# Performance work log

Measured on AMD Instinct MI355X. Metric: run time of the kernel, lower is better.

Reference implementation:

```python
import jax, jax.numpy as jnp
import numpy as np

# Config (matches init_kwargs)
N, P, K, DIMS = 16, 1024, 16, 3
C_IN, C_MID, C_OUT, DM = 64, 64, 128, 4
C_CAT = C_MID + C_IN          # channels entering depthwise-separable conv
KK = K * K
BN_EPS = 1e-5


def setup_inputs() -> dict:
    key = jax.random.key(0)
    ks = jax.random.split(key, 24)
    s = 0.05  # small init scale for weights
    inp = {
        # forward args
        "rep_pt": jax.random.normal(ks[0], (N, P, DIMS), jnp.float32),
        "pts":    jax.random.normal(ks[1], (N, P, K, DIMS), jnp.float32),
        "fts":    jax.random.normal(ks[2], (N, P, K, C_IN), jnp.float32),
        # dense1 / dense2 (point lifting MLP), weights stored (in, out)
        "w1": jax.random.normal(ks[3], (DIMS, C_MID), jnp.float32) * s,
        "b1": jnp.zeros((C_MID,), jnp.float32),
        "w2": jax.random.normal(ks[4], (C_MID, C_MID), jnp.float32) * s,
        "b2": jnp.zeros((C_MID,), jnp.float32),
        # conv1: Conv2d(dims, K*K, (1,K)); weight (KK, dims, K)
        "wc1": jax.random.normal(ks[5], (KK, DIMS, K), jnp.float32) * s,
        "bc1": jnp.zeros((KK,), jnp.float32),
        # x_dense1 (ELU) and x_dense2 (no activation)
        "wx1": jax.random.normal(ks[6], (KK, KK), jnp.float32) * s,
        "bx1": jnp.zeros((KK,), jnp.float32),
        "wx2": jax.random.normal(ks[7], (KK, KK), jnp.float32) * s,
        "bx2": jnp.zeros((KK,), jnp.float32),
        # depthwise Conv2d(C_CAT, C_CAT*DM, (1,K), groups=C_CAT): weight (C_CAT, DM, K)
        "wdw": jax.random.normal(ks[8], (C_CAT, DM, K), jnp.float32) * s,
        "bdw": jnp.zeros((C_CAT * DM,), jnp.float32),
        # pointwise Conv2d(C_CAT*DM, C_OUT, 1): weight stored (C_CAT*DM, C_OUT)
        "wpw": jax.random.normal(ks[9], (C_CAT * DM, C_OUT), jnp.float32) * s,
        "bpw": jnp.zeros((C_OUT,), jnp.float32),
        # BatchNorm2d(C_OUT) in eval mode (running stats)
        "bn_gamma": jnp.ones((C_OUT,), jnp.float32),
        "bn_beta":  jnp.zeros((C_OUT,), jnp.float32),
        "bn_mean":  jax.random.normal(ks[10], (C_OUT,), jnp.float32) * 0.1,
        "bn_var":   jax.random.uniform(ks[11], (C_OUT,), jnp.float32, 0.5, 1.5),
    }
    return inp


def reference(rep_pt, pts, fts, w1, b1, w2, b2, wc1, bc1, wx1, bx1, wx2, bx2,
              wdw, bdw, wpw, bpw, bn_gamma, bn_beta, bn_mean, bn_var):
    elu = jax.nn.elu
    n, p, k = pts.shape[0], pts.shape[1], pts.shape[2]

    # localize points around representative point: (N,P,K,dims)
    pts_local = pts - rep_pt[:, :, None, :]

    # lift coordinates to C_mid features (two Dense+ELU)
    h = elu(pts_local @ w1 + b1)
    h = elu(h @ w2 + b2)
    fts_cat = jnp.concatenate([h, fts], axis=-1)  # (N,P,K,C_CAT)

    # learned X-transform: conv1 over the K neighbors -> (N,P,K*K)
    X = elu(jnp.einsum('npkd,odk->npo', pts_local, wc1) + bc1)
    X = elu(X @ wx1 + bx1)
    X = X @ wx2 + bx2            # x_dense2: no activation
    X = X.reshape(n, p, k, k)    # (N,P,K,K)

    # apply X-transform to concatenated features
    fts_X = jnp.einsum('npij,npjc->npic', X, fts_cat)  # (N,P,K,C_CAT)

    # depthwise conv (kernel (1,K), groups=C_CAT, depth multiplier DM)
    # torch grouped-conv channel order: out channel o = c*DM + d
    dw = jnp.einsum('npkc,cdk->npcd', fts_X, wdw).reshape(n, p, -1) + bdw
    # pointwise 1x1 conv -> C_OUT, then ELU
    y = elu(dw @ wpw + bpw)      # (N,P,C_OUT)
    # BatchNorm2d in eval mode (per-channel affine with running stats)
    y = (y - bn_mean) * (bn_gamma / jnp.sqrt(bn_var + BN_EPS)) + bn_beta
    return y                     # (N,P,C_OUT)
```

## Files before the change

### kernel.cpp

```cpp
#include <hip/hip_runtime.h>

#define NPTS 16384
#define MPB  16
#define NTHR 256
#define WS_NEEDED 401408u

typedef __attribute__((ext_vector_type(8))) short bf16x8;
typedef __attribute__((ext_vector_type(4))) float f32x4;

__device__ __forceinline__ unsigned short f2bf(float x) {
    unsigned u = __float_as_uint(x);
    return (unsigned short)((u + 0x7FFFu + ((u >> 16) & 1u)) >> 16);
}
__device__ __forceinline__ float bf2f(unsigned short h) {
    return __uint_as_float(((unsigned)h) << 16);
}
__device__ __forceinline__ float elu_f(float x) {
    return x > 0.f ? x : (__expf(x) - 1.f);
}

__device__ __forceinline__ bf16x8 load_bfrag(const float* __restrict__ W, int N,
                                             int kt, int nt, int lane) {
    int k0  = kt * 32 + ((lane >> 4) << 3);
    int col = nt * 16 + (lane & 15);
    const float* s = W + k0 * N + col;
    bf16x8 r;
#pragma unroll
    for (int j = 0; j < 8; j++) r[j] = (short)f2bf(s[j * N]);
    return r;
}

__global__ void pack_weights(const float* __restrict__ w2,
                             const float* __restrict__ wx1,
                             const float* __restrict__ wx2,
                             const float* __restrict__ wpw,
                             unsigned short* __restrict__ dst) {
    int gid  = blockIdx.x * 256 + threadIdx.x;
    int frag = gid >> 6, lane = gid & 63;
    const float* src; int N, fl;
    if      (frag <   8) { src = w2;  N =  64; fl = frag;       }
    else if (frag < 136) { src = wx1; N = 256; fl = frag - 8;   }
    else if (frag < 264) { src = wx2; N = 256; fl = frag - 136; }
    else                 { src = wpw; N = 128; fl = frag - 264; }
    int NT  = N >> 4;
    int kt  = fl / NT, nt = fl - kt * NT;
    int k0  = kt * 32 + (lane >> 4) * 8;
    int col = nt * 16 + (lane & 15);
    const float* s = src + k0 * N + col;
    unsigned v[4];
#pragma unroll
    for (int u = 0; u < 4; u++) {
        unsigned lo = f2bf(s[(2 * u) * N]);
        unsigned hi = f2bf(s[(2 * u + 1) * N]);
        v[u] = lo | (hi << 16);
    }
    *(uint4*)&dst[gid * 8] = make_uint4(v[0], v[1], v[2], v[3]);
}

template <bool PACKED>
__global__ __launch_bounds__(NTHR, 2)
void xconv_main(const float* __restrict__ rep_pt, const float* __restrict__ pts,
                const float* __restrict__ fts,
                const float* __restrict__ w1,  const float* __restrict__ b1,
                const float* __restrict__ w2,  const float* __restrict__ b2,
                const float* __restrict__ wc1, const float* __restrict__ bc1,
                const float* __restrict__ wx1, const float* __restrict__ bx1,
                const float* __restrict__ wx2, const float* __restrict__ bx2,
                const float* __restrict__ wdw, const float* __restrict__ bdw,
                const float* __restrict__ wpw, const float* __restrict__ bpw,
                const float* __restrict__ bn_gamma, const float* __restrict__ bn_beta,
                const float* __restrict__ bn_mean,  const float* __restrict__ bn_var,
                const unsigned short* __restrict__ wpack,
                float* __restrict__ out) {
    __shared__ __align__(16) char smem[62720];
    float*          s_ptsl = (float*)smem;
    unsigned short* s_h2   = (unsigned short*)(smem + 3072);
    unsigned short* s_h1   = (unsigned short*)(smem + 35840);
    unsigned short* s_x0   = (unsigned short*)(smem + 35840);
    unsigned short* s_x1   = (unsigned short*)(smem + 44288);
    unsigned short* s_dw   = (unsigned short*)(smem + 35840);
    unsigned short* s_x2   = (unsigned short*)(smem + 54272);

    const int t    = threadIdx.x;
    const int lane = t & 63;
    const int w    = t >> 6;
    const int gp0  = blockIdx.x * MPB;

    for (int idx = t; idx < MPB * 48; idx += NTHR) {
        int m = idx / 48, r = idx - m * 48;
        int k = r / 3,    d = r - k * 3;
        int gp = gp0 + m;
        s_ptsl[idx] = pts[(gp * 16 + k) * 3 + d] - rep_pt[gp * 3 + d];
    }
    __syncthreads();

    for (int R = 0; R < 2; R++) {
        {
            int lr  = t >> 1;
            int row = 128 * R + lr;
            int m = row >> 4, k = row & 15;
            float p0 = s_ptsl[m * 48 + k * 3 + 0];
            float p1 = s_ptsl[m * 48 + k * 3 + 1];
            float p2 = s_ptsl[m * 48 + k * 3 + 2];
            int cb = (t & 1) * 32;
#pragma unroll
            for (int cc = 0; cc < 4; cc++) {
                unsigned v[4];
#pragma unroll
                for (int u = 0; u < 4; u++) {
                    int c0 = cb + cc * 8 + u * 2;
                    float a  = fmaf(p0, w1[c0],       fmaf(p1, w1[64 + c0],     fmaf(p2, w1[128 + c0],     b1[c0])));
                    float bb = fmaf(p0, w1[c0 + 1],   fmaf(p1, w1[64 + c0 + 1], fmaf(p2, w1[128 + c0 + 1], b1[c0 + 1])));
                    v[u] = (unsigned)f2bf(elu_f(a)) | ((unsigned)f2bf(elu_f(bb)) << 16);
                }
                *(uint4*)&s_h1[lr * 72 + cb + cc * 8] = make_uint4(v[0], v[1], v[2], v[3]);
            }
        }
        __syncthreads();
        {
            const bf16x8* wp = (const bf16x8*)wpack;
            bf16x8 Bf[8];
#pragma unroll
            for (int f = 0; f < 8; f++) {
                if (PACKED) Bf[f] = wp[f * 64 + lane];
                else        Bf[f] = load_bfrag(w2, 64, f >> 2, f & 3, lane);
            }
            float bias[4];
#pragma unroll
            for (int nt = 0; nt < 4; nt++) bias[nt] = b2[nt * 16 + (lane & 15)];
#pragma unroll
            for (int i = 0; i < 2; i++) {
                int rtl = w * 2 + i;
                int g0  = (8 * R + rtl) * 16;
                bf16x8 a0 = *(const bf16x8*)&s_h1[(rtl * 16 + (lane & 15)) * 72 + 0  + (lane >> 4) * 8];
                bf16x8 a1 = *(const bf16x8*)&s_h1[(rtl * 16 + (lane & 15)) * 72 + 32 + (lane >> 4) * 8];
#pragma unroll
                for (int nt = 0; nt < 4; nt++) {
                    f32x4 acc = {bias[nt], bias[nt], bias[nt], bias[nt]};
                    acc = __builtin_amdgcn_mfma_f32_16x16x32_bf16(a0, Bf[0 * 4 + nt], acc, 0, 0, 0);
                    acc = __builtin_amdgcn_mfma_f32_16x16x32_bf16(a1, Bf[1 * 4 + nt], acc, 0, 0, 0);
#pragma unroll
                    for (int r = 0; r < 4; r++) {
                        int krow = (lane >> 4) * 4 + r;
                        s_h2[(g0 + krow) * 64 + nt * 16 + (lane & 15)] = f2bf(elu_f(acc[r]));
                    }
                }
            }
        }
        __syncthreads();
    }

    {
        float wreg[48];
#pragma unroll
        for (int q = 0; q < 12; q++) {
            float4 wv = *(const float4*)&wc1[t * 48 + q * 4];
            wreg[q * 4 + 0] = wv.x; wreg[q * 4 + 1] = wv.y;
            wreg[q * 4 + 2] = wv.z; wreg[q * 4 + 3] = wv.w;
        }
        float bo = bc1[t];
#pragma unroll 1
        for (int m = 0; m < MPB; m++) {
            float acc = bo;
#pragma unroll
            for (int q = 0; q < 12; q++) {
                float4 pv = *(const float4*)&s_ptsl[m * 48 + q * 4];
                acc = fmaf(pv.x, wreg[((q * 4 + 0) % 3) * 16 + (q * 4 + 0) / 3], acc);
                acc = fmaf(pv.y, wreg[((q * 4 + 1) % 3) * 16 + (q * 4 + 1) / 3], acc);
                acc = fmaf(pv.z, wreg[((q * 4 + 2) % 3) * 16 + (q * 4 + 2) / 3], acc);
                acc = fmaf(pv.w, wreg[((q * 4 + 3) % 3) * 16 + (q * 4 + 3) / 3], acc);
            }
            s_x0[m * 264 + t] = f2bf(elu_f(acc));
        }
    }
    __syncthreads();

    {
        const bf16x8* wp = (const bf16x8*)wpack + 512;
        f32x4 acc[4];
#pragma unroll
        for (int q = 0; q < 4; q++) {
            float bv = bx1[(w * 4 + q) * 16 + (lane & 15)];
            acc[q] = (f32x4){bv, bv, bv, bv};
        }
#pragma unroll
        for (int kt = 0; kt < 8; kt++) {
            bf16x8 a = *(const bf16x8*)&s_x0[(lane & 15) * 264 + kt * 32 + (lane >> 4) * 8];
#pragma unroll
            for (int q = 0; q < 4; q++) {
                int nt = w * 4 + q;
                bf16x8 b;
                if (PACKED) b = wp[(kt * 16 + nt) * 64 + lane];
                else        b = load_bfrag(wx1, 256, kt, nt, lane);
                acc[q] = __builtin_amdgcn_mfma_f32_16x16x32_bf16(a, b, acc[q], 0, 0, 0);
            }
        }
#pragma unroll
        for (int q = 0; q < 4; q++) {
            int nt = w * 4 + q;
#pragma unroll
            for (int r = 0; r < 4; r++) {
                int m = (lane >> 4) * 4 + r;
                s_x1[m * 264 + nt * 16 + (lane & 15)] = f2bf(elu_f(acc[q][r]));
            }
        }
    }
    __syncthreads();

    {
        const bf16x8* wp = (const bf16x8*)wpack + 8704;
        f32x4 acc[4];
#pragma unroll
        for (int q = 0; q < 4; q++) {
            float bv = bx2[(w * 4 + q) * 16 + (lane & 15)];
            acc[q] = (f32x4){bv, bv, bv, bv};
        }
#pragma unroll
        for (int kt = 0; kt < 8; kt++) {
            bf16x8 a = *(const bf16x8*)&s_x1[(lane & 15) * 264 + kt * 32 + (lane >> 4) * 8];
#pragma unroll
            for (int q = 0; q < 4; q++) {
                int nt = w * 4 + q;
                bf16x8 b;
                if (PACKED) b = wp[(kt * 16 + nt) * 64 + lane];
                else        b = load_bfrag(wx2, 256, kt, nt, lane);
                acc[q] = __builtin_amdgcn_mfma_f32_16x16x32_bf16(a, b, acc[q], 0, 0, 0);
            }
        }
#pragma unroll
        for (int q = 0; q < 4; q++) {
            int nt = w * 4 + q;
#pragma unroll
            for (int r = 0; r < 4; r++) {
                int m = (lane >> 4) * 4 + r;
                s_x2[m * 264 + nt * 16 + (lane & 15)] = f2bf(acc[q][r]);
            }
        }
    }
    __syncthreads();

    {
        const int c  = t & 127;
        const int mg = t >> 7;
        float wd[64];
#pragma unroll
        for (int q = 0; q < 16; q++) {
            float4 v = *(const float4*)&wdw[c * 64 + q * 4];
            wd[q * 4 + 0] = v.x; wd[q * 4 + 1] = v.y;
            wd[q * 4 + 2] = v.z; wd[q * 4 + 3] = v.w;
        }
        float bd[4];
#pragma unroll
        for (int d = 0; d < 4; d++) bd[d] = bdw[c * 4 + d];
#pragma unroll 1
        for (int ml = 0; ml < 8; ml++) {
            int m  = mg * 8 + ml;
            int gp = gp0 + m;
            float fc[16];
            if (c < 64) {
#pragma unroll
                for (int j = 0; j < 16; j++) fc[j] = bf2f(s_h2[(m * 16 + j) * 64 + c]);
            } else {
#pragma unroll
                for (int j = 0; j < 16; j++) fc[j] = fts[(gp * 16 + j) * 64 + (c - 64)];
            }
            float fXr[16];
#pragma unroll
            for (int i = 0; i < 16; i++) {
                float a = 0.f;
#pragma unroll
                for (int jj = 0; jj < 2; jj++) {
                    uint4 xv = *(const uint4*)&s_x2[m * 264 + i * 16 + jj * 8];
                    a = fmaf(__uint_as_float(xv.x << 16),          fc[jj * 8 + 0], a);
                    a = fmaf(__uint_as_float(xv.x & 0xFFFF0000u),  fc[jj * 8 + 1], a);
                    a = fmaf(__uint_as_float(xv.y << 16),          fc[jj * 8 + 2], a);
                    a = fmaf(__uint_as_float(xv.y & 0xFFFF0000u),  fc[jj * 8 + 3], a);
                    a = fmaf(__uint_as_float(xv.z << 16),          fc[jj * 8 + 4], a);
                    a = fmaf(__uint_as_float(xv.z & 0xFFFF0000u),  fc[jj * 8 + 5], a);
                    a = fmaf(__uint_as_float(xv.w << 16),          fc[jj * 8 + 6], a);
                    a = fmaf(__uint_as_float(xv.w & 0xFFFF0000u),  fc[jj * 8 + 7], a);
                }
                fXr[i] = a;
            }
            ushort4 dv;
            {
                float o[4];
#pragma unroll
                for (int d = 0; d < 4; d++) {
                    float a = bd[d];
#pragma unroll
                    for (int k = 0; k < 16; k++) a = fmaf(fXr[k], wd[d * 16 + k], a);
                    o[d] = a;
                }
                dv.x = f2bf(o[0]); dv.y = f2bf(o[1]); dv.z = f2bf(o[2]); dv.w = f2bf(o[3]);
            }
            *(ushort4*)&s_dw[m * 520 + c * 4] = dv;
        }
    }
    __syncthreads();

    {
        const bf16x8* wp = (const bf16x8*)wpack + 16896;
        f32x4 acc[2];
#pragma unroll
        for (int q = 0; q < 2; q++) {
            float bv = bpw[(w * 2 + q) * 16 + (lane & 15)];
            acc[q] = (f32x4){bv, bv, bv, bv};
        }
#pragma unroll
        for (int kt = 0; kt < 16; kt++) {
            bf16x8 a = *(const bf16x8*)&s_dw[(lane & 15) * 520 + kt * 32 + (lane >> 4) * 8];
#pragma unroll
            for (int q = 0; q < 2; q++) {
                int nt = w * 2 + q;
                bf16x8 b;
                if (PACKED) b = wp[(kt * 8 + nt) * 64 + lane];
                else        b = load_bfrag(wpw, 128, kt, nt, lane);
                acc[q] = __builtin_amdgcn_mfma_f32_16x16x32_bf16(a, b, acc[q], 0, 0, 0);
            }
        }
#pragma unroll
        for (int q = 0; q < 2; q++) {
            int co = (w * 2 + q) * 16 + (lane & 15);
            float scale = bn_gamma[co] * rsqrtf(bn_var[co] + 1e-5f);
            float shift = bn_beta[co] - bn_mean[co] * scale;
#pragma unroll
            for (int r = 0; r < 4; r++) {
                int m = (lane >> 4) * 4 + r;
                out[(gp0 + m) * 128 + co] = fmaf(elu_f(acc[q][r]), scale, shift);
            }
        }
    }
}

extern "C" void kernel_launch(void* const* d_in, const int* in_sizes, int n_in,
                              void* d_out, int out_size, void* d_ws, size_t ws_size,
                              hipStream_t stream) {
    const float* rep_pt   = (const float*)d_in[0];
    const float* pts      = (const float*)d_in[1];
    const float* fts      = (const float*)d_in[2];
    const float* w1       = (const float*)d_in[3];
    const float* b1       = (const float*)d_in[4];
    const float* w2       = (const float*)d_in[5];
    const float* b2       = (const float*)d_in[6];
    const float* wc1      = (const float*)d_in[7];
    const float* bc1      = (const float*)d_in[8];
    const float* wx1      = (const float*)d_in[9];
    const float* bx1      = (const float*)d_in[10];
    const float* wx2      = (const float*)d_in[11];
    const float* bx2      = (const float*)d_in[12];
    const float* wdw      = (const float*)d_in[13];
    const float* bdw      = (const float*)d_in[14];
    const float* wpw      = (const float*)d_in[15];
    const float* bpw      = (const float*)d_in[16];
    const float* bn_gamma = (const float*)d_in[17];
    const float* bn_beta  = (const float*)d_in[18];
    const float* bn_mean  = (const float*)d_in[19];
    const float* bn_var   = (const float*)d_in[20];
    float* out = (float*)d_out;

    const bool packed = (d_ws != nullptr) && (ws_size >= (size_t)WS_NEEDED);
    unsigned short* wpack = (unsigned short*)d_ws;

    if (packed) {
        pack_weights<<<98, 256, 0, stream>>>(w2, wx1, wx2, wpw, wpack);
        xconv_main<true><<<NPTS / MPB, NTHR, 0, stream>>>(
            rep_pt, pts, fts, w1, b1, w2, b2, wc1, bc1, wx1, bx1, wx2, bx2,
            wdw, bdw, wpw, bpw, bn_gamma, bn_beta, bn_mean, bn_var, wpack, out);
    } else {
        xconv_main<false><<<NPTS / MPB, NTHR, 0, stream>>>(
            rep_pt, pts, fts, w1, b1, w2, b2, wc1, bc1, wx1, bx1, wx2, bx2,
            wdw, bdw, wpw, bpw, bn_gamma, bn_beta, bn_mean, bn_var, (const unsigned short*)nullptr, out);
    }
}
```

Baseline: 205.5 us.

## Double block size to 512 threads and drop separate weight-packing kernel

Raises threads per block from 256 to 512 and splits every stage (MLP lift, conv1, x_dense MFMAs, depthwise, pointwise) across 8 waves, so each wave handles fewer tiles. It removes the pre-pass kernel that packed weights into bf16 MFMA fragments and instead converts fp32 weights to bf16 inline on each load, which saves a launch but repeats strided global loads and conversions in every block. Launch bounds move to (512,4), which caps register use per thread. Shared memory stays at about 62 KB, so only two blocks fit per CU, and the bound mostly affects spilling risk.

After: 233.1 us. 13.4% more time.

```diff
diff --git a/kernel.cpp b/kernel.cpp
--- a/kernel.cpp
+++ b/kernel.cpp
@@ -2,8 +2,7 @@
 
 #define NPTS 16384
 #define MPB  16
-#define NTHR 256
-#define WS_NEEDED 401408u
+#define NTHR 512
 
 typedef __attribute__((ext_vector_type(8))) short bf16x8;
 typedef __attribute__((ext_vector_type(4))) float f32x4;
@@ -11,6 +10,11 @@
 __device__ __forceinline__ unsigned short f2bf(float x) {
     unsigned u = __float_as_uint(x);
     return (unsigned short)((u + 0x7FFFu + ((u >> 16) & 1u)) >> 16);
+}
+__device__ __forceinline__ unsigned pack2(float a, float b) {
+    unsigned ua = __float_as_uint(a), ub = __float_as_uint(b);
+    return ((ua + 0x7FFFu + ((ua >> 16) & 1u)) >> 16) |
+           ((ub + 0x7FFFu + ((ub >> 16) & 1u)) & 0xFFFF0000u);
 }
 __device__ __forceinline__ float bf2f(unsigned short h) {
     return __uint_as_float(((unsigned)h) << 16);
@@ -24,41 +28,13 @@
     int k0  = kt * 32 + ((lane >> 4) << 3);
     int col = nt * 16 + (lane & 15);
     const float* s = W + k0 * N + col;
-    bf16x8 r;
-#pragma unroll
-    for (int j = 0; j < 8; j++) r[j] = (short)f2bf(s[j * N]);
-    return r;
-}
-
-__global__ void pack_weights(const float* __restrict__ w2,
-                             const float* __restrict__ wx1,
-                             const float* __restrict__ wx2,
-                             const float* __restrict__ wpw,
-                             unsigned short* __restrict__ dst) {
-    int gid  = blockIdx.x * 256 + threadIdx.x;
-    int frag = gid >> 6, lane = gid & 63;
-    const float* src; int N, fl;
-    if      (frag <   8) { src = w2;  N =  64; fl = frag;       }
-    else if (frag < 136) { src = wx1; N = 256; fl = frag - 8;   }
-    else if (frag < 264) { src = wx2; N = 256; fl = frag - 136; }
-    else                 { src = wpw; N = 128; fl = frag - 264; }
-    int NT  = N >> 4;
-    int kt  = fl / NT, nt = fl - kt * NT;
-    int k0  = kt * 32 + (lane >> 4) * 8;
-    int col = nt * 16 + (lane & 15);
-    const float* s = src + k0 * N + col;
-    unsigned v[4];
-#pragma unroll
-    for (int u = 0; u < 4; u++) {
-        unsigned lo = f2bf(s[(2 * u) * N]);
-        unsigned hi = f2bf(s[(2 * u + 1) * N]);
-        v[u] = lo | (hi << 16);
-    }
-    *(uint4*)&dst[gid * 8] = make_uint4(v[0], v[1], v[2], v[3]);
-}
-
-template <bool PACKED>
-__global__ __launch_bounds__(NTHR, 2)
+    union { bf16x8 v; unsigned u[4]; } r;
+#pragma unroll
+    for (int j = 0; j < 4; j++) r.u[j] = pack2(s[(2 * j) * N], s[(2 * j + 1) * N]);
+    return r.v;
+}
+
+__global__ __launch_bounds__(NTHR, 4)
 void xconv_main(const float* __restrict__ rep_pt, const float* __restrict__ pts,
                 const float* __restrict__ fts,
                 const float* __restrict__ w1,  const float* __restrict__ b1,
@@ -70,7 +46,6 @@
                 const float* __restrict__ wpw, const float* __restrict__ bpw,
                 const float* __restrict__ bn_gamma, const float* __restrict__ bn_beta,
                 const float* __restrict__ bn_mean,  const float* __restrict__ bn_var,
-                const unsigned short* __restrict__ wpack,
                 float* __restrict__ out) {
     __shared__ __align__(16) char smem[62720];
     float*          s_ptsl = (float*)smem;
@@ -84,6 +59,8 @@
     const int t    = threadIdx.x;
     const int lane = t & 63;
     const int w    = t >> 6;
+    const int c0   = lane & 15;
+    const int q    = lane >> 4;
     const int gp0  = blockIdx.x * MPB;
 
     for (int idx = t; idx < MPB * 48; idx += NTHR) {
@@ -94,146 +71,136 @@
     }
     __syncthreads();
 
-    for (int R = 0; R < 2; R++) {
-        {
-            int lr  = t >> 1;
-            int row = 128 * R + lr;
-            int m = row >> 4, k = row & 15;
-            float p0 = s_ptsl[m * 48 + k * 3 + 0];
-            float p1 = s_ptsl[m * 48 + k * 3 + 1];
-            float p2 = s_ptsl[m * 48 + k * 3 + 2];
-            int cb = (t & 1) * 32;
-#pragma unroll
-            for (int cc = 0; cc < 4; cc++) {
-                unsigned v[4];
-#pragma unroll
-                for (int u = 0; u < 4; u++) {
-                    int c0 = cb + cc * 8 + u * 2;
-                    float a  = fmaf(p0, w1[c0],       fmaf(p1, w1[64 + c0],     fmaf(p2, w1[128 + c0],     b1[c0])));
-                    float bb = fmaf(p0, w1[c0 + 1],   fmaf(p1, w1[64 + c0 + 1], fmaf(p2, w1[128 + c0 + 1], b1[c0 + 1])));
-                    v[u] = (unsigned)f2bf(elu_f(a)) | ((unsigned)f2bf(elu_f(bb)) << 16);
+    {
+        bf16x8 Bf[8];
+#pragma unroll
+        for (int f = 0; f < 8; f++) Bf[f] = load_bfrag(w2, 64, f >> 2, f & 3, lane);
+        float b2v[4];
+#pragma unroll
+        for (int nt = 0; nt < 4; nt++) b2v[nt] = b2[nt * 16 + c0];
+
+        for (int R = 0; R < 2; R++) {
+            {
+                int lr  = t >> 2;
+                int row = 128 * R + lr;
+                int m = row >> 4, k = row & 15;
+                float p0 = s_ptsl[m * 48 + k * 3 + 0];
+                float p1 = s_ptsl[m * 48 + k * 3 + 1];
+                float p2 = s_ptsl[m * 48 + k * 3 + 2];
+                int cb = (t & 3) * 16;
+#pragma unroll
+                for (int cc = 0; cc < 2; cc++) {
+                    unsigned v[4];
+#pragma unroll
+                    for (int u = 0; u < 4; u++) {
+                        int ci = cb + cc * 8 + u * 2;
+                        float a  = fmaf(p0, w1[ci],     fmaf(p1, w1[64 + ci],     fmaf(p2, w1[128 + ci],     b1[ci])));
+                        float bb = fmaf(p0, w1[ci + 1], fmaf(p1, w1[64 + ci + 1], fmaf(p2, w1[128 + ci + 1], b1[ci + 1])));
+                        v[u] = pack2(elu_f(a), elu_f(bb));
+                    }
+                    *(uint4*)&s_h1[lr * 72 + cb + cc * 8] = make_uint4(v[0], v[1], v[2], v[3]);
                 }
-                *(uint4*)&s_h1[lr * 72 + cb + cc * 8] = make_uint4(v[0], v[1], v[2], v[3]);
-            }
-        }
-        __syncthreads();
-        {
-            const bf16x8* wp = (const bf16x8*)wpack;
-            bf16x8 Bf[8];
-#pragma unroll
-            for (int f = 0; f < 8; f++) {
-                if (PACKED) Bf[f] = wp[f * 64 + lane];
-                else        Bf[f] = load_bfrag(w2, 64, f >> 2, f & 3, lane);
-            }
-            float bias[4];
-#pragma unroll
-            for (int nt = 0; nt < 4; nt++) bias[nt] = b2[nt * 16 + (lane & 15)];
-#pragma unroll
-            for (int i = 0; i < 2; i++) {
-                int rtl = w * 2 + i;
-                int g0  = (8 * R + rtl) * 16;
-                bf16x8 a0 = *(const bf16x8*)&s_h1[(rtl * 16 + (lane & 15)) * 72 + 0  + (lane >> 4) * 8];
-                bf16x8 a1 = *(const bf16x8*)&s_h1[(rtl * 16 + (lane & 15)) * 72 + 32 + (lane >> 4) * 8];
+            }
+            __syncthreads();
+            {
+                int g0 = (8 * R + w) * 16;
+                bf16x8 a0 = *(const bf16x8*)&s_h1[(w * 16 + c0) * 72 + 0  + q * 8];
+                bf16x8 a1 = *(const bf16x8*)&s_h1[(w * 16 + c0) * 72 + 32 + q * 8];
 #pragma unroll
                 for (int nt = 0; nt < 4; nt++) {
-                    f32x4 acc = {bias[nt], bias[nt], bias[nt], bias[nt]};
-                    acc = __builtin_amdgcn_mfma_f32_16x16x32_bf16(a0, Bf[0 * 4 + nt], acc, 0, 0, 0);
-                    acc = __builtin_amdgcn_mfma_f32_16x16x32_bf16(a1, Bf[1 * 4 + nt], acc, 0, 0, 0);
+                    f32x4 acc = {b2v[nt], b2v[nt], b2v[nt], b2v[nt]};
+                    acc = __builtin_amdgcn_mfma_f32_16x16x32_bf16(a0, Bf[nt],     acc, 0, 0, 0);
+                    acc = __builtin_amdgcn_mfma_f32_16x16x32_bf16(a1, Bf[4 + nt], acc, 0, 0, 0);
 #pragma unroll
                     for (int r = 0; r < 4; r++) {
-                        int krow = (lane >> 4) * 4 + r;
-                        s_h2[(g0 + krow) * 64 + nt * 16 + (lane & 15)] = f2bf(elu_f(acc[r]));
+                        int krow = q * 4 + r;
+                        s_h2[(g0 + krow) * 64 + nt * 16 + c0] = f2bf(elu_f(acc[r]));
                     }
                 }
             }
-        }
-        __syncthreads();
-    }
-
-    {
+            __syncthreads();
+        }
+    }
+
+    {
+        int o    = t & 255;
+        int half = t >> 8;
         float wreg[48];
 #pragma unroll
-        for (int q = 0; q < 12; q++) {
-            float4 wv = *(const float4*)&wc1[t * 48 + q * 4];
-            wreg[q * 4 + 0] = wv.x; wreg[q * 4 + 1] = wv.y;
-            wreg[q * 4 + 2] = wv.z; wreg[q * 4 + 3] = wv.w;
-        }
-        float bo = bc1[t];
+        for (int qq = 0; qq < 12; qq++) {
+            float4 wv = *(const float4*)&wc1[o * 48 + qq * 4];
+            wreg[qq * 4 + 0] = wv.x; wreg[qq * 4 + 1] = wv.y;
+            wreg[qq * 4 + 2] = wv.z; wreg[qq * 4 + 3] = wv.w;
+        }
+        float bo = bc1[o];
 #pragma unroll 1
-        for (int m = 0; m < MPB; m++) {
+        for (int mm = 0; mm < 8; mm++) {
+            int m = half * 8 + mm;
             float acc = bo;
 #pragma unroll
-            for (int q = 0; q < 12; q++) {
-                float4 pv = *(const float4*)&s_ptsl[m * 48 + q * 4];
-                acc = fmaf(pv.x, wreg[((q * 4 + 0) % 3) * 16 + (q * 4 + 0) / 3], acc);
-                acc = fmaf(pv.y, wreg[((q * 4 + 1) % 3) * 16 + (q * 4 + 1) / 3], acc);
-                acc = fmaf(pv.z, wreg[((q * 4 + 2) % 3) * 16 + (q * 4 + 2) / 3], acc);
-                acc = fmaf(pv.w, wreg[((q * 4 + 3) % 3) * 16 + (q * 4 + 3) / 3], acc);
-            }
-            s_x0[m * 264 + t] = f2bf(elu_f(acc));
-        }
-    }
-    __syncthreads();
-
-    {
-        const bf16x8* wp = (const bf16x8*)wpack + 512;
-        f32x4 acc[4];
-#pragma unroll
-        for (int q = 0; q < 4; q++) {
-            float bv = bx1[(w * 4 + q) * 16 + (lane & 15)];
-            acc[q] = (f32x4){bv, bv, bv, bv};
+            for (int qq = 0; qq < 12; qq++) {
+                float4 pv = *(const float4*)&s_ptsl[m * 48 + qq * 4];
+                acc = fmaf(pv.x, wreg[((qq * 4 + 0) % 3) * 16 + (qq * 4 + 0) / 3], acc);
+                acc = fmaf(pv.y, wreg[((qq * 4 + 1) % 3) * 16 + (qq * 4 + 1) / 3], acc);
+                acc = fmaf(pv.z, wreg[((qq * 4 + 2) % 3) * 16 + (qq * 4 + 2) / 3], acc);
+                acc = fmaf(pv.w, wreg[((qq * 4 + 3) % 3) * 16 + (qq * 4 + 3) / 3], acc);
+            }
+            s_x0[m * 264 + o] = f2bf(elu_f(acc));
+        }
+    }
+    __syncthreads();
+
+    {
+        f32x4 acc[2];
+#pragma unroll
+        for (int p = 0; p < 2; p++) {
+            float bv = bx1[(w * 2 + p) * 16 + c0];
+            acc[p] = (f32x4){bv, bv, bv, bv};
         }
 #pragma unroll
         for (int kt = 0; kt < 8; kt++) {
-            bf16x8 a = *(const bf16x8*)&s_x0[(lane & 15) * 264 + kt * 32 + (lane >> 4) * 8];
-#pragma unroll
-            for (int q = 0; q < 4; q++) {
-                int nt = w * 4 + q;
-                bf16x8 b;
-                if (PACKED) b = wp[(kt * 16 + nt) * 64 + lane];
-                else        b = load_bfrag(wx1, 256, kt, nt, lane);
-                acc[q] = __builtin_amdgcn_mfma_f32_16x16x32_bf16(a, b, acc[q], 0, 0, 0);
-            }
-        }
-#pragma unroll
-        for (int q = 0; q < 4; q++) {
-            int nt = w * 4 + q;
+            bf16x8 a = *(const bf16x8*)&s_x0[c0 * 264 + kt * 32 + q * 8];
+#pragma unroll
+            for (int p = 0; p < 2; p++) {
+                bf16x8 b = load_bfrag(wx1, 256, kt, w * 2 + p, lane);
+                acc[p] = __builtin_amdgcn_mfma_f32_16x16x32_bf16(a, b, acc[p], 0, 0, 0);
+            }
+        }
+#pragma unroll
+        for (int p = 0; p < 2; p++) {
+            int nt = w * 2 + p;
 #pragma unroll
             for (int r = 0; r < 4; r++) {
-                int m = (lane >> 4) * 4 + r;
-                s_x1[m * 264 + nt * 16 + (lane & 15)] = f2bf(elu_f(acc[q][r]));
-            }
-        }
-    }
-    __syncthreads();
-
-    {
-        const bf16x8* wp = (const bf16x8*)wpack + 8704;
-        f32x4 acc[4];
-#pragma unroll
-        for (int q = 0; q < 4; q++) {
-            float bv = bx2[(w * 4 + q) * 16 + (lane & 15)];
-            acc[q] = (f32x4){bv, bv, bv, bv};
+                int m = q * 4 + r;
+                s_x1[m * 264 + nt * 16 + c0] = f2bf(elu_f(acc[p][r]));
+            }
+        }
+    }
+    __syncthreads();
+
+    {
+        f32x4 acc[2];
+#pragma unroll
+        for (int p = 0; p < 2; p++) {
+            float bv = bx2[(w * 2 + p) * 16 + c0];
+            acc[p] = (f32x4){bv, bv, bv, bv};
         }
 #pragma unroll
         for (int kt = 0; kt < 8; kt++) {
-            bf16x8 a = *(const bf16x8*)&s_x1[(lane & 15) * 264 + kt * 32 + (lane >> 4) * 8];
-#pragma unroll
-            for (int q = 0; q < 4; q++) {
-                int nt = w * 4 + q;
-                bf16x8 b;
-                if (PACKED) b = wp[(kt * 16 + nt) * 64 + lane];
-                else        b = load_bfrag(wx2, 256, kt, nt, lane);
-                acc[q] = __builtin_amdgcn_mfma_f32_16x16x32_bf16(a, b, acc[q], 0, 0, 0);
-            }
-        }
-#pragma unroll
-        for (int q = 0; q < 4; q++) {
-            int nt = w * 4 + q;
+            bf16x8 a = *(const bf16x8*)&s_x1[c0 * 264 + kt * 32 + q * 8];
+#pragma unroll
+            for (int p = 0; p < 2; p++) {
+                bf16x8 b = load_bfrag(wx2, 256, kt, w * 2 + p, lane);
+                acc[p] = __builtin_amdgcn_mfma_f32_16x16x32_bf16(a, b, acc[p], 0, 0, 0);
+            }
+        }
+#pragma unroll
+        for (int p = 0; p < 2; p++) {
+            int nt = w * 2 + p;
 #pragma unroll
             for (int r = 0; r < 4; r++) {
-                int m = (lane >> 4) * 4 + r;
-                s_x2[m * 264 + nt * 16 + (lane & 15)] = f2bf(acc[q][r]);
+                int m = q * 4 + r;
+                s_x2[m * 264 + nt * 16 + c0] = f2bf(acc[p][r]);
             }
         }
     }
@@ -244,17 +211,17 @@
         const int mg = t >> 7;
         float wd[64];
 #pragma unroll
-        for (int q = 0; q < 16; q++) {
-            float4 v = *(const float4*)&wdw[c * 64 + q * 4];
-            wd[q * 4 + 0] = v.x; wd[q * 4 + 1] = v.y;
-            wd[q * 4 + 2] = v.z; wd[q * 4 + 3] = v.w;
+        for (int qq = 0; qq < 16; qq++) {
+            float4 v = *(const float4*)&wdw[c * 64 + qq * 4];
+            wd[qq * 4 + 0] = v.x; wd[qq * 4 + 1] = v.y;
+            wd[qq * 4 + 2] = v.z; wd[qq * 4 + 3] = v.w;
         }
         float bd[4];
 #pragma unroll
         for (int d = 0; d < 4; d++) bd[d] = bdw[c * 4 + d];
 #pragma unroll 1
-        for (int ml = 0; ml < 8; ml++) {
-            int m  = mg * 8 + ml;
+        for (int ml = 0; ml < 4; ml++) {
+            int m  = mg * 4 + ml;
             int gp = gp0 + m;
             float fc[16];
             if (c < 64) {
@@ -300,35 +267,21 @@
     __syncthreads();
 
     {
-        const bf16x8* wp = (const bf16x8*)wpack + 16896;
-        f32x4 acc[2];
-#pragma unroll
-        for (int q = 0; q < 2; q++) {
-            float bv = bpw[(w * 2 + q) * 16 + (lane & 15)];
-            acc[q] = (f32x4){bv, bv, bv, bv};
-        }
+        float bv = bpw[w * 16 + c0];
+        f32x4 acc = {bv, bv, bv, bv};
 #pragma unroll
         for (int kt = 0; kt < 16; kt++) {
-            bf16x8 a = *(const bf16x8*)&s_dw[(lane & 15) * 520 + kt * 32 + (lane >> 4) * 8];
-#pragma unroll
-            for (int q = 0; q < 2; q++) {
-                int nt = w * 2 + q;
-                bf16x8 b;
-                if (PACKED) b = wp[(kt * 8 + nt) * 64 + lane];
-                else        b = load_bfrag(wpw, 128, kt, nt, lane);
-                acc[q] = __builtin_amdgcn_mfma_f32_16x16x32_bf16(a, b, acc[q], 0, 0, 0);
-            }
-        }
-#pragma unroll
-        for (int q = 0; q < 2; q++) {
-            int co = (w * 2 + q) * 16 + (lane & 15);
-            float scale = bn_gamma[co] * rsqrtf(bn_var[co] + 1e-5f);
-            float shift = bn_beta[co] - bn_mean[co] * scale;
-#pragma unroll
-            for (int r = 0; r < 4; r++) {
-                int m = (lane >> 4) * 4 + r;
-                out[(gp0 + m) * 128 + co] = fmaf(elu_f(acc[q][r]), scale, shift);
-            }
+            bf16x8 a = *(const bf16x8*)&s_dw[c0 * 520 + kt * 32 + q * 8];
+            bf16x8 b = load_bfrag(wpw, 128, kt, w, lane);
+            acc = __builtin_amdgcn_mfma_f32_16x16x32_bf16(a, b, acc, 0, 0, 0);
+        }
+        int co = w * 16 + c0;
+        float scale = bn_gamma[co] * rsqrtf(bn_var[co] + 1e-5f);
+        float shift = bn_beta[co] - bn_mean[co] * scale;
+#pragma unroll
+        for (int r = 0; r < 4; r++) {
+            int m = q * 4 + r;
+            out[(size_t)(gp0 + m) * 128 + co] = fmaf(elu_f(acc[r]), scale, shift);
         }
     }
 }
@@ -359,17 +312,7 @@
     const float* bn_var   = (const float*)d_in[20];
     float* out = (float*)d_out;
 
-    const bool packed = (d_ws != nullptr) && (ws_size >= (size_t)WS_NEEDED);
-    unsigned short* wpack = (unsigned short*)d_ws;
-
-    if (packed) {
-        pack_weights<<<98, 256, 0, stream>>>(w2, wx1, wx2, wpw, wpack);
-        xconv_main<true><<<NPTS / MPB, NTHR, 0, stream>>>(
-            rep_pt, pts, fts, w1, b1, w2, b2, wc1, bc1, wx1, bx1, wx2, bx2,
-            wdw, bdw, wpw, bpw, bn_gamma, bn_beta, bn_mean, bn_var, wpack, out);
-    } else {
-        xconv_main<false><<<NPTS / MPB, NTHR, 0, stream>>>(
-            rep_pt, pts, fts, w1, b1, w2, b2, wc1, bc1, wx1, bx1, wx2, bx2,
-            wdw, bdw, wpw, bpw, bn_gamma, bn_beta, bn_mean, bn_var, (const unsigned short*)nullptr, out);
-    }
-}
+    xconv_main<<<NPTS / MPB, NTHR, 0, stream>>>(
+        rep_pt, pts, fts, w1, b1, w2, b2, wc1, bc1, wx1, bx1, wx2, bx2,
+        wdw, bdw, wpw, bpw, bn_gamma, bn_beta, bn_mean, bn_var, out);
+}
```
